# Kernel optimization log

Hardware: AMD Instinct MI355X
Metric: run time of the kernel (lower is better)

The kernel has to match this reference:

```python
import jax, jax.numpy as jnp
import numpy as np

C = 256  # in_dims
CQ = C // 2


def setup_inputs() -> dict:
    key = jax.random.key(0)
    ks = jax.random.split(key, 8)
    B, H, W = 8, 64, 64
    x = jax.random.normal(ks[0], (B, C, H, W), dtype=jnp.float32)
    s = 0.02
    Wq = jax.random.normal(ks[1], (CQ, C), dtype=jnp.float32) * s
    bq = jax.random.normal(ks[2], (CQ,), dtype=jnp.float32) * s
    Wk = jax.random.normal(ks[3], (CQ, C), dtype=jnp.float32) * s
    bk = jax.random.normal(ks[4], (CQ,), dtype=jnp.float32) * s
    Wv = jax.random.normal(ks[5], (C, C), dtype=jnp.float32) * s
    bv = jax.random.normal(ks[6], (C,), dtype=jnp.float32) * s
    gamma = jax.random.normal(ks[7], (1,), dtype=jnp.float32) * 0.5  # torch inits to 0; use nonzero for a meaningful test
    return {"x": x, "Wq": Wq, "bq": bq, "Wk": Wk, "bk": bk, "Wv": Wv, "bv": bv, "gamma": gamma}


def reference(x, Wq, bq, Wk, bk, Wv, bv, gamma):
    B, Ch, H, W = x.shape
    N = H * W
    xf = x.reshape(B, Ch, N)  # 1x1 conv == per-pixel linear over channels
    q = jnp.einsum('oc,bcn->bon', Wq, xf) + bq[None, :, None]  # [B, C/2, N]
    k = jnp.einsum('oc,bcn->bon', Wk, xf) + bk[None, :, None]  # [B, C/2, N]
    v = jnp.einsum('oc,bcn->bon', Wv, xf) + bv[None, :, None]  # [B, C,   N]
    # attention[b, m, n] = q_m . k_n ; softmax over dim=1 (the m axis), matching nn.Softmax(dim=1)
    scores = jnp.einsum('bcm,bcn->bmn', q, k)  # [B, N, N]
    attn = jax.nn.softmax(scores, axis=1)
    # torch.bmm(V, A^T)[b,c,m] = sum_n V[b,c,n] * A[b,m,n]
    out = jnp.einsum('bcn,bmn->bcm', v, attn)  # [B, C, N]
    return gamma * out.reshape(B, Ch, H, W) + x
```

## Files before the change

### kernel.cpp

```cpp
#include <hip/hip_runtime.h>


typedef unsigned short u16;
typedef __attribute__((ext_vector_type(8))) short bf16x8;
typedef __attribute__((ext_vector_type(4))) short bf16x4;
typedef __attribute__((ext_vector_type(4))) float f32x4;

__device__ __forceinline__ float bf2f(u16 u) {
  union { unsigned int i; float f; } v; v.i = ((unsigned int)u) << 16; return v.f;
}
__device__ __forceinline__ u16 f2bf(float f) {
  union { float f; unsigned int i; } v; v.f = f;
  unsigned int r = v.i + 0x7fffu + ((v.i >> 16) & 1u);
  return (u16)(r >> 16);
}

#define NB 8
#define NC 256
#define NCQ 128
#define NN 4096
#define LOG2E 1.4426950408889634f

__device__ __forceinline__ int scan_bad(const u16* p, int ns, int tid) {
  int bad = 0;
  for (int i = tid; i < ns; i += 256) {
    const int e = (p[2 * i] >> 7) & 0xff;
    bad |= (e >= 0x90) ? 1 : 0;
  }
  return bad;
}

__device__ __forceinline__ bf16x8 load8(const u16* pb, const float* pf,
                                        size_t off, bool f) {
  if (!f) return *(const bf16x8*)(pb + off);
  const float4 a = *(const float4*)(pf + off);
  const float4 b = *(const float4*)(pf + off + 4);
  bf16x8 r;
  r[0] = (short)f2bf(a.x); r[1] = (short)f2bf(a.y);
  r[2] = (short)f2bf(a.z); r[3] = (short)f2bf(a.w);
  r[4] = (short)f2bf(b.x); r[5] = (short)f2bf(b.y);
  r[6] = (short)f2bf(b.z); r[7] = (short)f2bf(b.w);
  return r;
}

__global__ __launch_bounds__(256, 2) void qkv_kernel(
    const void* xv, const void* Wqv, const void* bqv, const void* Wkv,
    const void* bkv, const void* Wvv, const void* bvv,
    u16* __restrict__ q2T, u16* __restrict__ kT, u16* __restrict__ vout) {
  __shared__ __align__(16) u16 xT[64][264];
  __shared__ int fl[8];
  const int tid = threadIdx.x;
  const int bid = blockIdx.x;
  const int b = bid & 7, n0 = (bid >> 3) << 6;

  if (tid < 8) fl[tid] = 0;
  __syncthreads();
  if (scan_bad((const u16*)xv, 256, tid)) fl[0] = 1;
  if (scan_bad((const u16*)Wqv, 64, tid)) fl[1] = 1;
  if (scan_bad((const u16*)Wkv, 64, tid)) fl[2] = 1;
  if (scan_bad((const u16*)Wvv, 64, tid)) fl[3] = 1;
  if (scan_bad((const u16*)bqv, 64, tid)) fl[4] = 1;
  if (scan_bad((const u16*)bkv, 64, tid)) fl[5] = 1;
  if (scan_bad((const u16*)bvv, 64, tid)) fl[6] = 1;
  __syncthreads();
  const bool fx = fl[0] != 0;

  {
    const int c = tid;
    const size_t roff = (size_t)(b * NC + c) * NN + n0;
    if (fx) {
      const float* xp = (const float*)xv + roff;
#pragma unroll
      for (int j = 0; j < 16; ++j) {
        const float4 t = *(const float4*)(xp + j * 4);
        xT[j * 4 + 0][c] = f2bf(t.x); xT[j * 4 + 1][c] = f2bf(t.y);
        xT[j * 4 + 2][c] = f2bf(t.z); xT[j * 4 + 3][c] = f2bf(t.w);
      }
    } else {
      const u16* xp = (const u16*)xv + roff;
#pragma unroll
      for (int j = 0; j < 8; ++j) {
        bf16x8 t = *(const bf16x8*)(xp + j * 8);
#pragma unroll
        for (int e = 0; e < 8; ++e) xT[j * 8 + e][c] = (u16)t[e];
      }
    }
  }
  __syncthreads();

  const int w = tid >> 6, lane = tid & 63, l15 = lane & 15, quad = lane >> 4;
  const u16* Wb; const float* Wf; const u16* Bb; const float* Bf;
  bool fW, fB; int obase = 0; u16* dstT = nullptr; float sc = 1.f;
  if (w == 0) {
    Wb = (const u16*)Wqv; Wf = (const float*)Wqv;
    Bb = (const u16*)bqv; Bf = (const float*)bqv;
    fW = fl[1]; fB = fl[4]; dstT = q2T; sc = LOG2E;
  } else if (w == 1) {
    Wb = (const u16*)Wkv; Wf = (const float*)Wkv;
    Bb = (const u16*)bkv; Bf = (const float*)bkv;
    fW = fl[2]; fB = fl[5]; dstT = kT;
  } else if (w == 2) {
    Wb = (const u16*)Wvv; Wf = (const float*)Wvv;
    Bb = (const u16*)bvv; Bf = (const float*)bvv;
    fW = fl[3]; fB = fl[6];
  } else {
    Wb = (const u16*)Wvv + 32768; Wf = (const float*)Wvv + 32768;
    Bb = (const u16*)bvv + 128;   Bf = (const float*)bvv + 128;
    fW = fl[3]; fB = fl[6]; obase = 128;
  }

  bf16x8 xfr[4][8];
#pragma unroll
  for (int nt = 0; nt < 4; ++nt) {
    const u16* xp = &xT[nt * 16 + l15][quad * 8];
#pragma unroll
    for (int ks = 0; ks < 8; ++ks) xfr[nt][ks] = *(const bf16x8*)(xp + ks * 32);
  }

  for (int ot = 0; ot < 8; ++ot) {
    bf16x8 wfr[8];
    const size_t wrow = (size_t)(ot * 16 + l15) * 256 + quad * 8;
#pragma unroll
    for (int ks = 0; ks < 8; ++ks) wfr[ks] = load8(Wb, Wf, wrow + ks * 32, fW);
    float bias[4];
    {
      const int boff = ot * 16 + quad * 4;
#pragma unroll
      for (int r = 0; r < 4; ++r)
        bias[r] = fB ? Bf[boff + r] : bf2f(Bb[boff + r]);
    }
#pragma unroll
    for (int nt = 0; nt < 4; ++nt) {
      f32x4 acc = {0.f, 0.f, 0.f, 0.f};
#pragma unroll
      for (int ks = 0; ks < 8; ++ks)
        acc = __builtin_amdgcn_mfma_f32_16x16x32_bf16(wfr[ks], xfr[nt][ks], acc, 0, 0, 0);
      const int n = n0 + nt * 16 + l15;
      if (w < 2) {
        ushort4 st;
        st.x = f2bf((acc[0] + bias[0]) * sc); st.y = f2bf((acc[1] + bias[1]) * sc);
        st.z = f2bf((acc[2] + bias[2]) * sc); st.w = f2bf((acc[3] + bias[3]) * sc);
        *(ushort4*)(dstT + ((size_t)(b * NN + n)) * NCQ + ot * 16 + quad * 4) = st;
      } else {
        const int c = obase + ot * 16 + quad * 4;
#pragma unroll
        for (int r = 0; r < 4; ++r)
          vout[((size_t)(b * NC + c + r)) * NN + n] = f2bf(acc[r] + bias[r]);
      }
    }
  }
}

__global__ __launch_bounds__(512, 4) void stats_kernel(
    const u16* __restrict__ q2T, const u16* __restrict__ kT,
    float* __restrict__ rbuf) {
  __shared__ float zbuf[8][64];
  const int bid = blockIdx.x;
  const int b = bid & 7, n0 = (bid >> 3) << 6;
  const int tid = threadIdx.x;
  const int w = tid >> 6, lane = tid & 63, l15 = lane & 15, quad = lane >> 4;

  bf16x8 kf[4][4];
  {
    const u16* kp = kT + ((size_t)(b * NN + n0 + l15)) * NCQ + quad * 8;
#pragma unroll
    for (int nt = 0; nt < 4; ++nt)
#pragma unroll
      for (int ks = 0; ks < 4; ++ks) {
        kf[nt][ks] = *(const bf16x8*)(kp + (size_t)(nt * 16) * NCQ + ks * 32);
        asm volatile("" : "+v"(kf[nt][ks]));
      }
  }

  const u16* qbase = q2T + ((size_t)(b * NN + w * 512 + l15)) * NCQ + quad * 8;
  float Z[4] = {0.f, 0.f, 0.f, 0.f};
  for (int it = 0; it < 32; ++it) {
    const u16* qp = qbase + (size_t)(it * 16) * NCQ;
    bf16x8 af[4];
#pragma unroll
    for (int ks = 0; ks < 4; ++ks) af[ks] = *(const bf16x8*)(qp + ks * 32);
#pragma unroll
    for (int nt = 0; nt < 4; ++nt) {
      f32x4 acc = {0.f, 0.f, 0.f, 0.f};
#pragma unroll
      for (int ks = 0; ks < 4; ++ks)
        acc = __builtin_amdgcn_mfma_f32_16x16x32_bf16(af[ks], kf[nt][ks], acc, 0, 0, 0);
      Z[nt] += __builtin_amdgcn_exp2f(acc[0]) + __builtin_amdgcn_exp2f(acc[1]) +
               __builtin_amdgcn_exp2f(acc[2]) + __builtin_amdgcn_exp2f(acc[3]);
    }
  }
#pragma unroll
  for (int nt = 0; nt < 4; ++nt) {
    float z = Z[nt];
    z += __shfl_xor(z, 16, 64);
    z += __shfl_xor(z, 32, 64);
    Z[nt] = z;
  }
  if (lane < 16) {
#pragma unroll
    for (int nt = 0; nt < 4; ++nt) zbuf[w][nt * 16 + lane] = Z[nt];
  }
  __syncthreads();
  if (tid < 64) {
    float z = 0.f;
#pragma unroll
    for (int ww = 0; ww < 8; ++ww) z += zbuf[ww][tid];
    rbuf[b * NN + n0 + tid] = 1.0f / z;
  }
}

__global__ __launch_bounds__(256, 4) void scale_kernel(
    u16* __restrict__ vr, const float* __restrict__ rbuf) {
  const int flat = (blockIdx.x * 256 + threadIdx.x) * 8;
  const int n = flat & (NN - 1);
  const int b = flat >> 20;
  const float4 r0 = *(const float4*)(rbuf + (b << 12) + n);
  const float4 r1 = *(const float4*)(rbuf + (b << 12) + n + 4);
  const ushort4 a0 = *(const ushort4*)(vr + flat);
  const ushort4 a1 = *(const ushort4*)(vr + flat + 4);
  ushort4 s0, s1;
  s0.x = f2bf(bf2f(a0.x) * r0.x); s0.y = f2bf(bf2f(a0.y) * r0.y);
  s0.z = f2bf(bf2f(a0.z) * r0.z); s0.w = f2bf(bf2f(a0.w) * r0.w);
  s1.x = f2bf(bf2f(a1.x) * r1.x); s1.y = f2bf(bf2f(a1.y) * r1.y);
  s1.z = f2bf(bf2f(a1.z) * r1.z); s1.w = f2bf(bf2f(a1.w) * r1.w);
  *(ushort4*)(vr + flat) = s0;
  *(ushort4*)(vr + flat + 4) = s1;
}

__global__ __launch_bounds__(256, 6) void out_kernel(
    const u16* __restrict__ q2T, const u16* __restrict__ kT,
    const u16* __restrict__ vr,
    const void* xv, const void* gv,
    const void* bqv, const void* bkv, const void* bvv,
    void* outv) {
  __shared__ __align__(16) u16 qs[64][136];
  __shared__ __align__(16) u16 et[4][16][68];
  __shared__ int fl[2];
  const int tid = threadIdx.x;
  if (tid < 2) fl[tid] = 0;
  __syncthreads();
  if (scan_bad((const u16*)xv, 256, tid)) fl[0] = 1;
  if (scan_bad((const u16*)bqv, 64, tid) | scan_bad((const u16*)bkv, 64, tid) |
      scan_bad((const u16*)bvv, 64, tid)) fl[1] = 1;

  const int bid = blockIdx.x;
  const int b = bid & 7;
  const int r7 = bid >> 3;
  const int ch = r7 & 1;
  const int m0 = (r7 >> 1) << 6;
  const int w = tid >> 6, lane = tid & 63, l15 = lane & 15, quad = lane >> 4;

  {
    const int mm = tid >> 2, ck = (tid & 3) * 32;
    const u16* src = q2T + ((size_t)(b * NN + m0 + mm)) * NCQ + ck;
#pragma unroll
    for (int j = 0; j < 4; ++j)
      *(bf16x8*)(&qs[mm][ck + j * 8]) = *(const bf16x8*)(src + j * 8);
  }
  __syncthreads();
  const bool fx = fl[0] != 0, fg = fl[1] != 0;

  f32x4 acc[8];
#pragma unroll
  for (int i = 0; i < 8; ++i) acc[i] = (f32x4){0.f, 0.f, 0.f, 0.f};

  const u16* kb = kT + ((size_t)(b * NN + w * 16 + l15)) * NCQ + quad * 8;
  const u16* vb = vr + ((size_t)(b * NC + ch * 128 + w * 32 + l15)) * NN + quad * 8;

  for (int n0 = 0; n0 < NN; n0 += 64) {
    bf16x8 kf[4], vf[4];
#pragma unroll
    for (int ks = 0; ks < 4; ++ks)
      kf[ks] = *(const bf16x8*)(kb + (size_t)n0 * NCQ + ks * 32);
#pragma unroll
    for (int ct = 0; ct < 2; ++ct)
#pragma unroll
      for (int ns = 0; ns < 2; ++ns)
        vf[ct * 2 + ns] =
            *(const bf16x8*)(vb + (size_t)(ct * 16) * NN + n0 + ns * 32);
#pragma unroll
    for (int mg = 0; mg < 4; ++mg) {
      f32x4 s = {0.f, 0.f, 0.f, 0.f};
#pragma unroll
      for (int ks = 0; ks < 4; ++ks) {
        const bf16x8 qfr =
            *(const bf16x8*)(&qs[mg * 16 + l15][quad * 8 + ks * 32]);
        s = __builtin_amdgcn_mfma_f32_16x16x32_bf16(kf[ks], qfr, s, 0, 0, 0);
      }
      bf16x4 ev;
      ev[0] = (short)f2bf(__builtin_amdgcn_exp2f(s[0]));
      ev[1] = (short)f2bf(__builtin_amdgcn_exp2f(s[1]));
      ev[2] = (short)f2bf(__builtin_amdgcn_exp2f(s[2]));
      ev[3] = (short)f2bf(__builtin_amdgcn_exp2f(s[3]));
      *(bf16x4*)(&et[mg][l15][w * 16 + quad * 4]) = ev;
    }
    __syncthreads();
#pragma unroll
    for (int mg = 0; mg < 4; ++mg)
#pragma unroll
      for (int ns = 0; ns < 2; ++ns) {
        const bf16x8 af = *(const bf16x8*)(&et[mg][l15][ns * 32 + quad * 8]);
#pragma unroll
        for (int ct = 0; ct < 2; ++ct)
          acc[mg * 2 + ct] = __builtin_amdgcn_mfma_f32_16x16x32_bf16(
              af, vf[ct * 2 + ns], acc[mg * 2 + ct], 0, 0, 0);
      }
    __syncthreads();
  }

  const float g = fg ? ((const float*)gv)[0] : bf2f(((const u16*)gv)[0]);
#pragma unroll
  for (int mg = 0; mg < 4; ++mg)
#pragma unroll
    for (int ct = 0; ct < 2; ++ct) {
      const int c = ch * 128 + w * 32 + ct * 16 + l15;
      const int m = m0 + mg * 16 + quad * 4;
      const size_t base = ((size_t)(b * NC + c)) * NN + m;
      const f32x4 a = acc[mg * 2 + ct];
      if (fx) {
        const float4 xl = *(const float4*)((const float*)xv + base);
        float4 st;
        st.x = g * a[0] + xl.x; st.y = g * a[1] + xl.y;
        st.z = g * a[2] + xl.z; st.w = g * a[3] + xl.w;
        *(float4*)((float*)outv + base) = st;
      } else {
        const ushort4 xl = *(const ushort4*)((const u16*)xv + base);
        ushort4 st;
        st.x = f2bf(g * a[0] + bf2f(xl.x));
        st.y = f2bf(g * a[1] + bf2f(xl.y));
        st.z = f2bf(g * a[2] + bf2f(xl.z));
        st.w = f2bf(g * a[3] + bf2f(xl.w));
        *(ushort4*)((u16*)outv + base) = st;
      }
    }
}

extern "C" void kernel_launch(void* const* d_in, const int* in_sizes, int n_in,
                              void* d_out, int out_size, void* d_ws, size_t ws_size,
                              hipStream_t stream) {
  const size_t NEED = 33554432u;
  if (ws_size < NEED) return;

  char* ws = (char*)d_ws;
  u16* q2 = (u16*)(ws);
  u16* kk = (u16*)(ws + 8388608);
  u16* vv = (u16*)(ws + 16777216);
  float* rbuf = (ws_size >= NEED + 131072u) ? (float*)(ws + NEED) : (float*)d_out;

  qkv_kernel<<<512, 256, 0, stream>>>(d_in[0], d_in[1], d_in[2], d_in[3],
                                      d_in[4], d_in[5], d_in[6], q2, kk, vv);
  stats_kernel<<<512, 512, 0, stream>>>(q2, kk, rbuf);
  scale_kernel<<<4096, 256, 0, stream>>>(vv, rbuf);
  out_kernel<<<1024, 256, 0, stream>>>(q2, kk, vv, d_in[0], d_in[7],
                                       d_in[2], d_in[4], d_in[6], d_out);
}
```

Measured before the change: 437.1 us.

## Restructure attention output kernel to keep P in registers with split-N waves

The out kernel now lets each wave own a slice of the N (key) dimension and reuse the QK^T MFMA output layout directly as the operand of a 16x16x16 MFMA for P·V. This removes the per-iteration LDS round trip and the two block barriers in the main loop. Q fragments stay in registers, and the m tile shrinks to 32, which doubles the grid. The partial sums from the four waves are reduced serially through LDS at the end, and occupancy hints drop from 6 to 2 because of the larger accumulator register footprint.

```diff
diff --git a/kernel.cpp b/kernel.cpp
--- a/kernel.cpp
+++ b/kernel.cpp
@@ -13,6 +13,11 @@
   union { float f; unsigned int i; } v; v.f = f;
   unsigned int r = v.i + 0x7fffu + ((v.i >> 16) & 1u);
   return (u16)(r >> 16);
+}
+
+__device__ __forceinline__ f32x4 mfma16(bf16x4 a, bf16x4 b, f32x4 c) {
+  asm("v_mfma_f32_16x16x16_bf16 %0, %1, %2, %0" : "+v"(c) : "v"(a), "v"(b));
+  return c;
 }
 
 #define NB 8
@@ -227,14 +232,13 @@
   *(ushort4*)(vr + flat + 4) = s1;
 }
 
-__global__ __launch_bounds__(256, 6) void out_kernel(
+__global__ __launch_bounds__(256, 2) void out_kernel(
     const u16* __restrict__ q2T, const u16* __restrict__ kT,
     const u16* __restrict__ vr,
     const void* xv, const void* gv,
     const void* bqv, const void* bkv, const void* bvv,
     void* outv) {
-  __shared__ __align__(16) u16 qs[64][136];
-  __shared__ __align__(16) u16 et[4][16][68];
+  __shared__ float Obuf[32][132];
   __shared__ int fl[2];
   const int tid = threadIdx.x;
   if (tid < 2) fl[tid] = 0;
@@ -247,92 +251,119 @@
   const int b = bid & 7;
   const int r7 = bid >> 3;
   const int ch = r7 & 1;
-  const int m0 = (r7 >> 1) << 6;
+  const int m0 = (r7 >> 1) << 5;
   const int w = tid >> 6, lane = tid & 63, l15 = lane & 15, quad = lane >> 4;
 
+  bf16x8 qf[2][4];
   {
-    const int mm = tid >> 2, ck = (tid & 3) * 32;
-    const u16* src = q2T + ((size_t)(b * NN + m0 + mm)) * NCQ + ck;
-#pragma unroll
-    for (int j = 0; j < 4; ++j)
-      *(bf16x8*)(&qs[mm][ck + j * 8]) = *(const bf16x8*)(src + j * 8);
-  }
-  __syncthreads();
-  const bool fx = fl[0] != 0, fg = fl[1] != 0;
-
-  f32x4 acc[8];
-#pragma unroll
-  for (int i = 0; i < 8; ++i) acc[i] = (f32x4){0.f, 0.f, 0.f, 0.f};
+    const u16* qp = q2T + ((size_t)(b * NN + m0 + l15)) * NCQ + quad * 8;
+#pragma unroll
+    for (int mg = 0; mg < 2; ++mg)
+#pragma unroll
+      for (int ks = 0; ks < 4; ++ks) {
+        qf[mg][ks] = *(const bf16x8*)(qp + (size_t)(mg * 16) * NCQ + ks * 32);
+        asm volatile("" : "+v"(qf[mg][ks]));
+      }
+  }
+
+  f32x4 acc[2][8];
+#pragma unroll
+  for (int mg = 0; mg < 2; ++mg)
+#pragma unroll
+    for (int ct = 0; ct < 8; ++ct) acc[mg][ct] = (f32x4){0.f, 0.f, 0.f, 0.f};
 
   const u16* kb = kT + ((size_t)(b * NN + w * 16 + l15)) * NCQ + quad * 8;
-  const u16* vb = vr + ((size_t)(b * NC + ch * 128 + w * 32 + l15)) * NN + quad * 8;
-
+  const u16* vb = vr + ((size_t)(b * NC + ch * 128 + l15)) * NN + w * 16 + quad * 4;
+
+#pragma unroll 2
   for (int n0 = 0; n0 < NN; n0 += 64) {
-    bf16x8 kf[4], vf[4];
+    bf16x8 kf[4];
 #pragma unroll
     for (int ks = 0; ks < 4; ++ks)
       kf[ks] = *(const bf16x8*)(kb + (size_t)n0 * NCQ + ks * 32);
-#pragma unroll
-    for (int ct = 0; ct < 2; ++ct)
-#pragma unroll
-      for (int ns = 0; ns < 2; ++ns)
-        vf[ct * 2 + ns] =
-            *(const bf16x8*)(vb + (size_t)(ct * 16) * NN + n0 + ns * 32);
-#pragma unroll
-    for (int mg = 0; mg < 4; ++mg) {
+    bf16x4 vf[8];
+#pragma unroll
+    for (int ct = 0; ct < 8; ++ct)
+      vf[ct] = *(const bf16x4*)(vb + (size_t)(ct * 16) * NN + n0);
+    bf16x4 pf[2];
+#pragma unroll
+    for (int mg = 0; mg < 2; ++mg) {
       f32x4 s = {0.f, 0.f, 0.f, 0.f};
 #pragma unroll
-      for (int ks = 0; ks < 4; ++ks) {
-        const bf16x8 qfr =
-            *(const bf16x8*)(&qs[mg * 16 + l15][quad * 8 + ks * 32]);
-        s = __builtin_amdgcn_mfma_f32_16x16x32_bf16(kf[ks], qfr, s, 0, 0, 0);
-      }
+      for (int ks = 0; ks < 4; ++ks)
+        s = __builtin_amdgcn_mfma_f32_16x16x32_bf16(kf[ks], qf[mg][ks], s, 0, 0, 0);
       bf16x4 ev;
       ev[0] = (short)f2bf(__builtin_amdgcn_exp2f(s[0]));
       ev[1] = (short)f2bf(__builtin_amdgcn_exp2f(s[1]));
       ev[2] = (short)f2bf(__builtin_amdgcn_exp2f(s[2]));
       ev[3] = (short)f2bf(__builtin_amdgcn_exp2f(s[3]));
-      *(bf16x4*)(&et[mg][l15][w * 16 + quad * 4]) = ev;
-    }
-    __syncthreads();
-#pragma unroll
-    for (int mg = 0; mg < 4; ++mg)
-#pragma unroll
-      for (int ns = 0; ns < 2; ++ns) {
-        const bf16x8 af = *(const bf16x8*)(&et[mg][l15][ns * 32 + quad * 8]);
-#pragma unroll
-        for (int ct = 0; ct < 2; ++ct)
-          acc[mg * 2 + ct] = __builtin_amdgcn_mfma_f32_16x16x32_bf16(
-              af, vf[ct * 2 + ns], acc[mg * 2 + ct], 0, 0, 0);
-      }
-    __syncthreads();
-  }
-
+      pf[mg] = ev;
+    }
+#pragma unroll
+    for (int mg = 0; mg < 2; ++mg)
+#pragma unroll
+      for (int ct = 0; ct < 8; ++ct)
+        acc[mg][ct] = mfma16(vf[ct], pf[mg], acc[mg][ct]);
+  }
+
+  auto dump = [&](int add) {
+#pragma unroll
+    for (int mg = 0; mg < 2; ++mg)
+#pragma unroll
+      for (int ct = 0; ct < 8; ++ct) {
+        float* p = &Obuf[mg * 16 + l15][ct * 16 + quad * 4];
+        f32x4 t = acc[mg][ct];
+        if (add) {
+          const f32x4 o = *(const f32x4*)p;
+          t[0] += o[0]; t[1] += o[1]; t[2] += o[2]; t[3] += o[3];
+        }
+        *(f32x4*)p = t;
+      }
+  };
+  if (w == 0) dump(0);
+  __syncthreads();
+  if (w == 1) dump(1);
+  __syncthreads();
+  if (w == 2) dump(1);
+  __syncthreads();
+  if (w == 3) dump(1);
+  __syncthreads();
+
+  const bool fx = fl[0] != 0, fg = fl[1] != 0;
   const float g = fg ? ((const float*)gv)[0] : bf2f(((const u16*)gv)[0]);
-#pragma unroll
-  for (int mg = 0; mg < 4; ++mg)
-#pragma unroll
-    for (int ct = 0; ct < 2; ++ct) {
-      const int c = ch * 128 + w * 32 + ct * 16 + l15;
-      const int m = m0 + mg * 16 + quad * 4;
-      const size_t base = ((size_t)(b * NC + c)) * NN + m;
-      const f32x4 a = acc[mg * 2 + ct];
-      if (fx) {
-        const float4 xl = *(const float4*)((const float*)xv + base);
+  {
+    const int c = tid >> 1;
+    const int mh = (tid & 1) << 4;
+    float o[16];
+#pragma unroll
+    for (int j = 0; j < 16; ++j) o[j] = Obuf[mh + j][c];
+    const size_t base = ((size_t)(b * NC + ch * 128 + c)) * NN + m0 + mh;
+    if (fx) {
+      const float* xp = (const float*)xv + base;
+      float* op = (float*)outv + base;
+#pragma unroll
+      for (int jj = 0; jj < 4; ++jj) {
+        const float4 xl = *(const float4*)(xp + jj * 4);
         float4 st;
-        st.x = g * a[0] + xl.x; st.y = g * a[1] + xl.y;
-        st.z = g * a[2] + xl.z; st.w = g * a[3] + xl.w;
-        *(float4*)((float*)outv + base) = st;
-      } else {
-        const ushort4 xl = *(const ushort4*)((const u16*)xv + base);
+        st.x = g * o[jj * 4 + 0] + xl.x; st.y = g * o[jj * 4 + 1] + xl.y;
+        st.z = g * o[jj * 4 + 2] + xl.z; st.w = g * o[jj * 4 + 3] + xl.w;
+        *(float4*)(op + jj * 4) = st;
+      }
+    } else {
+      const u16* xp = (const u16*)xv + base;
+      u16* op = (u16*)outv + base;
+#pragma unroll
+      for (int jj = 0; jj < 4; ++jj) {
+        const ushort4 xl = *(const ushort4*)(xp + jj * 4);
         ushort4 st;
-        st.x = f2bf(g * a[0] + bf2f(xl.x));
-        st.y = f2bf(g * a[1] + bf2f(xl.y));
-        st.z = f2bf(g * a[2] + bf2f(xl.z));
-        st.w = f2bf(g * a[3] + bf2f(xl.w));
-        *(ushort4*)((u16*)outv + base) = st;
-      }
-    }
+        st.x = f2bf(g * o[jj * 4 + 0] + bf2f(xl.x));
+        st.y = f2bf(g * o[jj * 4 + 1] + bf2f(xl.y));
+        st.z = f2bf(g * o[jj * 4 + 2] + bf2f(xl.z));
+        st.w = f2bf(g * o[jj * 4 + 3] + bf2f(xl.w));
+        *(ushort4*)(op + jj * 4) = st;
+      }
+    }
+  }
 }
 
 extern "C" void kernel_launch(void* const* d_in, const int* in_sizes, int n_in,
@@ -351,6 +382,6 @@
                                       d_in[4], d_in[5], d_in[6], q2, kk, vv);
   stats_kernel<<<512, 512, 0, stream>>>(q2, kk, rbuf);
   scale_kernel<<<4096, 256, 0, stream>>>(vv, rbuf);
-  out_kernel<<<1024, 256, 0, stream>>>(q2, kk, vv, d_in[0], d_in[7],
+  out_kernel<<<2048, 256, 0, stream>>>(q2, kk, vv, d_in[0], d_in[7],
                                        d_in[2], d_in[4], d_in[6], d_out);
 }
```

Result: slower. 879.2 us (+101.1%).

## Widen attention-output blocks to all channels, double-buffer exp tile, pack bf16 converts

Applied to the files above, without the earlier changes.

The output kernel now runs 512-thread blocks that cover all 256 value channels for a 64-query tile. Previously two blocks each handled half the channels and both recomputed the same QK^T scores and exp. Each wave now computes half of the score groups for its key slice, so score MFMAs and exp2 per block are shared across all channels. The exp tile in LDS is double-buffered, which removes the trailing barrier per key step. The bf16 conversion uses packed v_cvt_pk_bf16_f32 inline asm. The trade-offs are larger blocks, fewer of them in the grid, and more register and LDS pressure.

```diff
diff --git a/kernel.cpp b/kernel.cpp
--- a/kernel.cpp
+++ b/kernel.cpp
@@ -13,6 +13,17 @@
   union { float f; unsigned int i; } v; v.f = f;
   unsigned int r = v.i + 0x7fffu + ((v.i >> 16) & 1u);
   return (u16)(r >> 16);
+}
+
+__device__ __forceinline__ bf16x4 exp2_pk4(f32x4 s) {
+  const float e0 = __builtin_amdgcn_exp2f(s[0]);
+  const float e1 = __builtin_amdgcn_exp2f(s[1]);
+  const float e2 = __builtin_amdgcn_exp2f(s[2]);
+  const float e3 = __builtin_amdgcn_exp2f(s[3]);
+  union { unsigned int u[2]; bf16x4 v; } r;
+  asm("v_cvt_pk_bf16_f32 %0, %1, %2" : "=v"(r.u[0]) : "v"(e0), "v"(e1));
+  asm("v_cvt_pk_bf16_f32 %0, %1, %2" : "=v"(r.u[1]) : "v"(e2), "v"(e3));
+  return r.v;
 }
 
 #define NB 8
@@ -227,14 +238,14 @@
   *(ushort4*)(vr + flat + 4) = s1;
 }
 
-__global__ __launch_bounds__(256, 6) void out_kernel(
+__global__ __launch_bounds__(512, 4) void out_kernel(
     const u16* __restrict__ q2T, const u16* __restrict__ kT,
     const u16* __restrict__ vr,
     const void* xv, const void* gv,
     const void* bqv, const void* bkv, const void* bvv,
     void* outv) {
   __shared__ __align__(16) u16 qs[64][136];
-  __shared__ __align__(16) u16 et[4][16][68];
+  __shared__ __align__(16) u16 et[2][4][16][68];
   __shared__ int fl[2];
   const int tid = threadIdx.x;
   if (tid < 2) fl[tid] = 0;
@@ -245,16 +256,15 @@
 
   const int bid = blockIdx.x;
   const int b = bid & 7;
-  const int r7 = bid >> 3;
-  const int ch = r7 & 1;
-  const int m0 = (r7 >> 1) << 6;
+  const int m0 = (bid >> 3) << 6;
   const int w = tid >> 6, lane = tid & 63, l15 = lane & 15, quad = lane >> 4;
+  const int mh = w >> 2, nq = w & 3;
 
   {
-    const int mm = tid >> 2, ck = (tid & 3) * 32;
+    const int mm = tid >> 3, ck = (tid & 7) * 16;
     const u16* src = q2T + ((size_t)(b * NN + m0 + mm)) * NCQ + ck;
 #pragma unroll
-    for (int j = 0; j < 4; ++j)
+    for (int j = 0; j < 2; ++j)
       *(bf16x8*)(&qs[mm][ck + j * 8]) = *(const bf16x8*)(src + j * 8);
   }
   __syncthreads();
@@ -264,10 +274,11 @@
 #pragma unroll
   for (int i = 0; i < 8; ++i) acc[i] = (f32x4){0.f, 0.f, 0.f, 0.f};
 
-  const u16* kb = kT + ((size_t)(b * NN + w * 16 + l15)) * NCQ + quad * 8;
-  const u16* vb = vr + ((size_t)(b * NC + ch * 128 + w * 32 + l15)) * NN + quad * 8;
+  const u16* kb = kT + ((size_t)(b * NN + nq * 16 + l15)) * NCQ + quad * 8;
+  const u16* vb = vr + ((size_t)(b * NC + w * 32 + l15)) * NN + quad * 8;
 
   for (int n0 = 0; n0 < NN; n0 += 64) {
+    const int pp = (n0 >> 6) & 1;
     bf16x8 kf[4], vf[4];
 #pragma unroll
     for (int ks = 0; ks < 4; ++ks)
@@ -279,33 +290,27 @@
         vf[ct * 2 + ns] =
             *(const bf16x8*)(vb + (size_t)(ct * 16) * NN + n0 + ns * 32);
 #pragma unroll
-    for (int mg = 0; mg < 4; ++mg) {
+    for (int mgl = 0; mgl < 2; ++mgl) {
       f32x4 s = {0.f, 0.f, 0.f, 0.f};
 #pragma unroll
       for (int ks = 0; ks < 4; ++ks) {
         const bf16x8 qfr =
-            *(const bf16x8*)(&qs[mg * 16 + l15][quad * 8 + ks * 32]);
+            *(const bf16x8*)(&qs[mh * 32 + mgl * 16 + l15][quad * 8 + ks * 32]);
         s = __builtin_amdgcn_mfma_f32_16x16x32_bf16(kf[ks], qfr, s, 0, 0, 0);
       }
-      bf16x4 ev;
-      ev[0] = (short)f2bf(__builtin_amdgcn_exp2f(s[0]));
-      ev[1] = (short)f2bf(__builtin_amdgcn_exp2f(s[1]));
-      ev[2] = (short)f2bf(__builtin_amdgcn_exp2f(s[2]));
-      ev[3] = (short)f2bf(__builtin_amdgcn_exp2f(s[3]));
-      *(bf16x4*)(&et[mg][l15][w * 16 + quad * 4]) = ev;
+      *(bf16x4*)(&et[pp][mh * 2 + mgl][l15][nq * 16 + quad * 4]) = exp2_pk4(s);
     }
     __syncthreads();
 #pragma unroll
     for (int mg = 0; mg < 4; ++mg)
 #pragma unroll
       for (int ns = 0; ns < 2; ++ns) {
-        const bf16x8 af = *(const bf16x8*)(&et[mg][l15][ns * 32 + quad * 8]);
+        const bf16x8 af = *(const bf16x8*)(&et[pp][mg][l15][ns * 32 + quad * 8]);
 #pragma unroll
         for (int ct = 0; ct < 2; ++ct)
           acc[mg * 2 + ct] = __builtin_amdgcn_mfma_f32_16x16x32_bf16(
               af, vf[ct * 2 + ns], acc[mg * 2 + ct], 0, 0, 0);
       }
-    __syncthreads();
   }
 
   const float g = fg ? ((const float*)gv)[0] : bf2f(((const u16*)gv)[0]);
@@ -313,7 +318,7 @@
   for (int mg = 0; mg < 4; ++mg)
 #pragma unroll
     for (int ct = 0; ct < 2; ++ct) {
-      const int c = ch * 128 + w * 32 + ct * 16 + l15;
+      const int c = w * 32 + ct * 16 + l15;
       const int m = m0 + mg * 16 + quad * 4;
       const size_t base = ((size_t)(b * NC + c)) * NN + m;
       const f32x4 a = acc[mg * 2 + ct];
@@ -351,6 +356,6 @@
                                       d_in[4], d_in[5], d_in[6], q2, kk, vv);
   stats_kernel<<<512, 512, 0, stream>>>(q2, kk, rbuf);
   scale_kernel<<<4096, 256, 0, stream>>>(vv, rbuf);
-  out_kernel<<<1024, 256, 0, stream>>>(q2, kk, vv, d_in[0], d_in[7],
-                                       d_in[2], d_in[4], d_in[6], d_out);
-}
+  out_kernel<<<512, 512, 0, stream>>>(q2, kk, vv, d_in[0], d_in[7],
+                                      d_in[2], d_in[4], d_in[6], d_out);
+}
```

Result: no change. 431.1 us (-1.4%).
